# Optimization experiments

Measured on AMD Instinct MI355X. Metric: run time of the kernel, lower is better.

Reference implementation:

```python
import jax, jax.numpy as jnp
import numpy as np

N, E = 100000, 400000
IN_C, OUT_C, EA_D = 64, 16, 8


def setup_inputs() -> dict:
    key = jax.random.key(0)
    ks = jax.random.split(key, 12)
    x = jax.random.normal(ks[0], (N, IN_C), dtype=jnp.float32)
    # row (target) indices generated in [1, N] because forward does row -= 1
    row = jax.random.randint(ks[1], (E,), 1, N + 1, dtype=jnp.int32)
    col = jax.random.randint(ks[2], (E,), 0, N, dtype=jnp.int32)
    edge_index = jnp.stack([row, col], axis=0)  # [2, E]
    edge_attr = jax.random.normal(ks[3], (E, EA_D), dtype=jnp.float32)
    s_in = 1.0 / np.sqrt(IN_C)
    s_ea = 1.0 / np.sqrt(EA_D)
    s_o = 1.0 / np.sqrt(OUT_C)
    lin_w = jax.random.uniform(ks[4], (IN_C, OUT_C), jnp.float32, -s_in, s_in)
    lin_b = jax.random.uniform(ks[5], (OUT_C,), jnp.float32, -s_in, s_in)
    ea_w = jax.random.uniform(ks[6], (EA_D, OUT_C), jnp.float32, -s_ea, s_ea)
    ea_b = jax.random.uniform(ks[7], (OUT_C,), jnp.float32, -s_ea, s_ea)
    attn_w1 = jax.random.uniform(ks[8], (OUT_C,), jnp.float32, -1.0, 1.0)  # Linear(1,out)
    attn_b1 = jax.random.uniform(ks[9], (OUT_C,), jnp.float32, -1.0, 1.0)
    attn_w2 = jax.random.uniform(ks[10], (OUT_C,), jnp.float32, -s_o, s_o)  # Linear(out,1)
    attn_b2 = jax.random.uniform(ks[11], (), jnp.float32, -s_o, s_o)
    return {"x": x, "edge_index": edge_index, "edge_attr": edge_attr,
            "lin_w": lin_w, "lin_b": lin_b, "ea_w": ea_w, "ea_b": ea_b,
            "attn_w1": attn_w1, "attn_b1": attn_b1, "attn_w2": attn_w2, "attn_b2": attn_b2}


def reference(x, edge_index, edge_attr, lin_w, lin_b, ea_w, ea_b,
              attn_w1, attn_b1, attn_w2, attn_b2):
    n = x.shape[0]
    h = x @ lin_w + lin_b                      # [N, out]
    row = edge_index[0] - 1                    # forward does row -= 1
    col = edge_index[1]
    ea = edge_attr @ ea_w + ea_b               # [E, out]
    agg = h[col] * ea                          # gather + elementwise  [E, out]
    # attn_mlp: per-scalar Linear(1,out)->ReLU->Linear(out,1) over last dim
    hid = jax.nn.relu(agg[..., None] * attn_w1 + attn_b1)  # [E, out, out]
    scores = hid @ attn_w2 + attn_b2           # [E, out]
    attn = jax.nn.softmax(scores, axis=1)      # softmax over channel dim
    agg = agg * attn
    out = jnp.zeros_like(h).at[row].add(agg)   # scatter_add over target nodes
    return out
```

## Files before the change

kernel.cpp:

```cpp
#include <hip/hip_runtime.h>

#define IN_C 64
#define OUT_C 16
#define EA_D 8

__device__ __forceinline__ void atomic_add_f32(float* p, float v) {
#if defined(__HIP_PLATFORM_AMD__) || defined(__AMDGCN__)
    unsafeAtomicAdd(p, v);
#else
    atomicAdd(p, v);
#endif
}

__global__ __launch_bounds__(256) void h_kernel(
    const float* __restrict__ x,
    const float* __restrict__ lin_w,
    const float* __restrict__ lin_b,
    float* __restrict__ h,
    float* __restrict__ out,
    int n)
{
    __shared__ float s_x [16][IN_C + 4];
    __shared__ float s_wt[16][IN_C + 4];

    const int t = threadIdx.x;
    const int nodeBase = blockIdx.x * 16;

    {
        const int idx = nodeBase * OUT_C + t;
        if (idx < n * OUT_C) out[idx] = 0.0f;
    }

    for (int i = t; i < IN_C * OUT_C; i += 256)
        s_wt[i & 15][i >> 4] = lin_w[i];

    {
        const int lr = t >> 4;
        const int k4 = (t & 15) * 4;
        const int node = nodeBase + lr;
        float4 v = make_float4(0.f, 0.f, 0.f, 0.f);
        if (node < n) v = *(const float4*)(x + (size_t)node * IN_C + k4);
        *(float4*)(&s_x[lr][k4]) = v;
    }
    __syncthreads();

    const int lr = t >> 4;
    const int c  = t & 15;
    const int node = nodeBase + lr;
    if (node < n) {
        float acc = lin_b[c];
        #pragma unroll
        for (int k4 = 0; k4 < IN_C; k4 += 4) {
            const float4 xv = *(const float4*)(&s_x [lr][k4]);
            const float4 wv = *(const float4*)(&s_wt[c ][k4]);
            acc = fmaf(xv.x, wv.x, acc);
            acc = fmaf(xv.y, wv.y, acc);
            acc = fmaf(xv.z, wv.z, acc);
            acc = fmaf(xv.w, wv.w, acc);
        }
        h[(size_t)node * OUT_C + c] = acc;
    }
}

__global__ __launch_bounds__(256) void edge_kernel(
    const int*   __restrict__ edge_index,
    const float* __restrict__ edge_attr,
    const float* __restrict__ ea_w,
    const float* __restrict__ ea_b,
    const float* __restrict__ w1,
    const float* __restrict__ b1,
    const float* __restrict__ w2,
    const float* __restrict__ b2,
    const float* __restrict__ h,
    float*       __restrict__ out,
    int E)
{
    __shared__ float s_eaw[EA_D * OUT_C];
    __shared__ float s_eab[OUT_C];

    const int t = threadIdx.x;
    if (t < EA_D * OUT_C)     s_eaw[t]       = ea_w[t];
    else if (t < 128 + OUT_C) s_eab[t - 128] = ea_b[t - 128];
    __syncthreads();

    const int gid = blockIdx.x * 256 + t;
    const int e = gid >> 4;
    const int c = gid & 15;
    if (e >= E) return;

    const int row = edge_index[e] - 1;
    const int col = edge_index[E + e];

    const float4* ap = (const float4*)(edge_attr + (size_t)e * EA_D);
    const float4 a0 = ap[0], a1 = ap[1];

    const float hv = h[(size_t)col * OUT_C + c];

    float d = s_eab[c];
    d = fmaf(a0.x, s_eaw[0 * OUT_C + c], d);
    d = fmaf(a0.y, s_eaw[1 * OUT_C + c], d);
    d = fmaf(a0.z, s_eaw[2 * OUT_C + c], d);
    d = fmaf(a0.w, s_eaw[3 * OUT_C + c], d);
    d = fmaf(a1.x, s_eaw[4 * OUT_C + c], d);
    d = fmaf(a1.y, s_eaw[5 * OUT_C + c], d);
    d = fmaf(a1.z, s_eaw[6 * OUT_C + c], d);
    d = fmaf(a1.w, s_eaw[7 * OUT_C + c], d);
    const float agg = hv * d;

    float s = b2[0];
    #pragma unroll
    for (int j = 0; j < OUT_C; ++j) {
        const float hm = fmaf(agg, w1[j], b1[j]);
        s = fmaf(fmaxf(hm, 0.0f), w2[j], s);
    }

    float mx = s;
    mx = fmaxf(mx, __shfl_xor(mx, 1));
    mx = fmaxf(mx, __shfl_xor(mx, 2));
    mx = fmaxf(mx, __shfl_xor(mx, 4));
    mx = fmaxf(mx, __shfl_xor(mx, 8));
    const float p = __expf(s - mx);
    float den = p;
    den += __shfl_xor(den, 1);
    den += __shfl_xor(den, 2);
    den += __shfl_xor(den, 4);
    den += __shfl_xor(den, 8);

    atomic_add_f32(out + (size_t)row * OUT_C + c, agg * (p / den));
}

extern "C" void kernel_launch(void* const* d_in, const int* in_sizes, int n_in,
                              void* d_out, int out_size, void* d_ws, size_t ws_size,
                              hipStream_t stream)
{
    const float* x          = (const float*)d_in[0];
    const int*   edge_index = (const int*)  d_in[1];
    const float* edge_attr  = (const float*)d_in[2];
    const float* lin_w      = (const float*)d_in[3];
    const float* lin_b      = (const float*)d_in[4];
    const float* ea_w       = (const float*)d_in[5];
    const float* ea_b       = (const float*)d_in[6];
    const float* attn_w1    = (const float*)d_in[7];
    const float* attn_b1    = (const float*)d_in[8];
    const float* attn_w2    = (const float*)d_in[9];
    const float* attn_b2    = (const float*)d_in[10];

    const int n = in_sizes[0] / IN_C;
    const int E = in_sizes[1] / 2;

    float* h   = (float*)d_ws;
    float* out = (float*)d_out;

    h_kernel<<<(n + 15) / 16, 256, 0, stream>>>(x, lin_w, lin_b, h, out, n);

    const long long threads = (long long)E * OUT_C;
    edge_kernel<<<(int)((threads + 255) / 256), 256, 0, stream>>>(
        edge_index, edge_attr, ea_w, ea_b,
        attn_w1, attn_b1, attn_w2, attn_b2,
        h, out, E);
}
```

Before: 131.0 us.

## Retile node projection to 64 nodes per block and use DPP softmax reductions

The node projection kernel now handles 64 nodes per block, and each thread computes four output channels. Weights are read through wave-uniform scalar loads instead of a transposed shared-memory copy. The edge kernel transposes the edge-attribute weights so each thread can read them as vectors, uses nontemporal loads for the edge streams, and replaces the shuffle-based max and sum reductions over 16 lanes with DPP row operations. The softmax division becomes a hardware reciprocal. The aim is to cut shared-memory traffic and cross-lane reduction cost, at a small risk to accuracy from the approximate reciprocal and to correctness from the DPP control choices.

```diff
diff --git a/kernel.cpp b/kernel.cpp
--- a/kernel.cpp
+++ b/kernel.cpp
@@ -3,6 +3,12 @@
 #define IN_C 64
 #define OUT_C 16
 #define EA_D 8
+
+typedef float f32x4 __attribute__((ext_vector_type(4)));
+
+#define DPPF(x, ctrl) \
+    __uint_as_float((unsigned)__builtin_amdgcn_update_dpp( \
+        0, (int)__float_as_uint(x), (ctrl), 0xF, 0xF, true))
 
 __device__ __forceinline__ void atomic_add_f32(float* p, float v) {
 #if defined(__HIP_PLATFORM_AMD__) || defined(__AMDGCN__)
@@ -20,46 +26,61 @@
     float* __restrict__ out,
     int n)
 {
-    __shared__ float s_x [16][IN_C + 4];
-    __shared__ float s_wt[16][IN_C + 4];
+    __shared__ float s_x[64][IN_C + 12];
 
     const int t = threadIdx.x;
-    const int nodeBase = blockIdx.x * 16;
+    const int nodeBase = blockIdx.x * 64;
 
     {
-        const int idx = nodeBase * OUT_C + t;
-        if (idx < n * OUT_C) out[idx] = 0.0f;
+        const int base = nodeBase * OUT_C + t;
+        const int lim = n * OUT_C;
+        #pragma unroll
+        for (int i = 0; i < 4; ++i) {
+            const int idx = base + 256 * i;
+            if (idx < lim) out[idx] = 0.0f;
+        }
     }
 
-    for (int i = t; i < IN_C * OUT_C; i += 256)
-        s_wt[i & 15][i >> 4] = lin_w[i];
-
     {
-        const int lr = t >> 4;
-        const int k4 = (t & 15) * 4;
-        const int node = nodeBase + lr;
-        float4 v = make_float4(0.f, 0.f, 0.f, 0.f);
-        if (node < n) v = *(const float4*)(x + (size_t)node * IN_C + k4);
-        *(float4*)(&s_x[lr][k4]) = v;
+        const int r  = t >> 4;
+        const int c4 = (t & 15) * 4;
+        #pragma unroll
+        for (int i = 0; i < 4; ++i) {
+            const int row = r + 16 * i;
+            const int node = nodeBase + row;
+            f32x4 v = {0.f, 0.f, 0.f, 0.f};
+            if (node < n) v = *(const f32x4*)(x + (size_t)node * IN_C + c4);
+            *(f32x4*)(&s_x[row][c4]) = v;
+        }
     }
     __syncthreads();
 
-    const int lr = t >> 4;
-    const int c  = t & 15;
-    const int node = nodeBase + lr;
-    if (node < n) {
-        float acc = lin_b[c];
+    const int node_l = t & 63;
+    const int cg = __builtin_amdgcn_readfirstlane(t >> 6);
+    const int c0 = cg * 4;
+    const int node = nodeBase + node_l;
+    if (node >= n) return;
+
+    float acc0 = lin_b[c0 + 0];
+    float acc1 = lin_b[c0 + 1];
+    float acc2 = lin_b[c0 + 2];
+    float acc3 = lin_b[c0 + 3];
+
+    #pragma unroll
+    for (int k = 0; k < IN_C; k += 4) {
+        const f32x4 xv = *(const f32x4*)(&s_x[node_l][k]);
         #pragma unroll
-        for (int k4 = 0; k4 < IN_C; k4 += 4) {
-            const float4 xv = *(const float4*)(&s_x [lr][k4]);
-            const float4 wv = *(const float4*)(&s_wt[c ][k4]);
-            acc = fmaf(xv.x, wv.x, acc);
-            acc = fmaf(xv.y, wv.y, acc);
-            acc = fmaf(xv.z, wv.z, acc);
-            acc = fmaf(xv.w, wv.w, acc);
+        for (int j = 0; j < 4; ++j) {
+            const float xs = xv[j];
+            const float* wr = lin_w + (k + j) * OUT_C + c0;
+            acc0 = fmaf(xs, wr[0], acc0);
+            acc1 = fmaf(xs, wr[1], acc1);
+            acc2 = fmaf(xs, wr[2], acc2);
+            acc3 = fmaf(xs, wr[3], acc3);
         }
-        h[(size_t)node * OUT_C + c] = acc;
     }
+    f32x4 res = {acc0, acc1, acc2, acc3};
+    *(f32x4*)(h + (size_t)node * OUT_C + c0) = res;
 }
 
 __global__ __launch_bounds__(256) void edge_kernel(
@@ -75,12 +96,12 @@
     float*       __restrict__ out,
     int E)
 {
-    __shared__ float s_eaw[EA_D * OUT_C];
+    __shared__ float s_eawT[16][12];
     __shared__ float s_eab[OUT_C];
 
     const int t = threadIdx.x;
-    if (t < EA_D * OUT_C)     s_eaw[t]       = ea_w[t];
-    else if (t < 128 + OUT_C) s_eab[t - 128] = ea_b[t - 128];
+    if (t < 128)                s_eawT[t & 15][t >> 4] = ea_w[(t >> 4) * OUT_C + (t & 15)];
+    else if (t < 128 + OUT_C)   s_eab[t - 128] = ea_b[t - 128];
     __syncthreads();
 
     const int gid = blockIdx.x * 256 + t;
@@ -88,23 +109,26 @@
     const int c = gid & 15;
     if (e >= E) return;
 
-    const int row = edge_index[e] - 1;
-    const int col = edge_index[E + e];
+    const int row = __builtin_nontemporal_load(edge_index + e) - 1;
+    const int col = __builtin_nontemporal_load(edge_index + E + e);
 
-    const float4* ap = (const float4*)(edge_attr + (size_t)e * EA_D);
-    const float4 a0 = ap[0], a1 = ap[1];
+    const f32x4* ap = (const f32x4*)(edge_attr + (size_t)e * EA_D);
+    const f32x4 a0 = __builtin_nontemporal_load(ap);
+    const f32x4 a1 = __builtin_nontemporal_load(ap + 1);
 
     const float hv = h[(size_t)col * OUT_C + c];
 
+    const f32x4 w0 = *(const f32x4*)(&s_eawT[c][0]);
+    const f32x4 w4 = *(const f32x4*)(&s_eawT[c][4]);
     float d = s_eab[c];
-    d = fmaf(a0.x, s_eaw[0 * OUT_C + c], d);
-    d = fmaf(a0.y, s_eaw[1 * OUT_C + c], d);
-    d = fmaf(a0.z, s_eaw[2 * OUT_C + c], d);
-    d = fmaf(a0.w, s_eaw[3 * OUT_C + c], d);
-    d = fmaf(a1.x, s_eaw[4 * OUT_C + c], d);
-    d = fmaf(a1.y, s_eaw[5 * OUT_C + c], d);
-    d = fmaf(a1.z, s_eaw[6 * OUT_C + c], d);
-    d = fmaf(a1.w, s_eaw[7 * OUT_C + c], d);
+    d = fmaf(a0.x, w0.x, d);
+    d = fmaf(a0.y, w0.y, d);
+    d = fmaf(a0.z, w0.z, d);
+    d = fmaf(a0.w, w0.w, d);
+    d = fmaf(a1.x, w4.x, d);
+    d = fmaf(a1.y, w4.y, d);
+    d = fmaf(a1.z, w4.z, d);
+    d = fmaf(a1.w, w4.w, d);
     const float agg = hv * d;
 
     float s = b2[0];
@@ -114,19 +138,22 @@
         s = fmaf(fmaxf(hm, 0.0f), w2[j], s);
     }
 
-    float mx = s;
-    mx = fmaxf(mx, __shfl_xor(mx, 1));
-    mx = fmaxf(mx, __shfl_xor(mx, 2));
-    mx = fmaxf(mx, __shfl_xor(mx, 4));
-    mx = fmaxf(mx, __shfl_xor(mx, 8));
-    const float p = __expf(s - mx);
+    float m = s;
+    m = fmaxf(m, DPPF(m, 0x140));
+    m = fmaxf(m, DPPF(m, 0x141));
+    m = fmaxf(m, DPPF(m, 0x4E));
+    m = fmaxf(m, DPPF(m, 0xB1));
+
+    const float p = __expf(s - m);
     float den = p;
-    den += __shfl_xor(den, 1);
-    den += __shfl_xor(den, 2);
-    den += __shfl_xor(den, 4);
-    den += __shfl_xor(den, 8);
+    den += DPPF(den, 0x140);
+    den += DPPF(den, 0x141);
+    den += DPPF(den, 0x4E);
+    den += DPPF(den, 0xB1);
 
-    atomic_add_f32(out + (size_t)row * OUT_C + c, agg * (p / den));
+    const float attn = p * __builtin_amdgcn_rcpf(den);
+
+    atomic_add_f32(out + (size_t)row * OUT_C + c, agg * attn);
 }
 
 extern "C" void kernel_launch(void* const* d_in, const int* in_sizes, int n_in,
@@ -151,7 +178,7 @@
     float* h   = (float*)d_ws;
     float* out = (float*)d_out;
 
-    h_kernel<<<(n + 15) / 16, 256, 0, stream>>>(x, lin_w, lin_b, h, out, n);
+    h_kernel<<<(n + 63) / 64, 256, 0, stream>>>(x, lin_w, lin_b, h, out, n);
 
     const long long threads = (long long)E * OUT_C;
     edge_kernel<<<(int)((threads + 255) / 256), 256, 0, stream>>>(
```

Result: slower. 138.6 us (+5.8%).
